# Optimization experiments

Measured on AMD Instinct MI355X. Metric: run time of the kernel, lower is better.

## Reference

```python
import jax, jax.numpy as jnp
import numpy as np

# Module config
SIZE = (2, 2)
B, H, W, C = 16, 64, 64, 256


def setup_inputs() -> dict:
    key = jax.random.key(0)
    updates = jax.random.normal(key, (B, H, W, C), dtype=jnp.float32)
    OH, OW = H * SIZE[0], W * SIZE[1]
    # argmax-style mask: flat index into [OH, OW, C] (per-batch), pointing at the
    # top-left element of each pooling window (structure of max_pool_with_argmax)
    h = jnp.arange(H, dtype=jnp.int64)[:, None, None] * SIZE[0]   # [H,1,1]
    w = jnp.arange(W, dtype=jnp.int64)[None, :, None] * SIZE[1]   # [1,W,1]
    c = jnp.arange(C, dtype=jnp.int64)[None, None, :]             # [1,1,C]
    mask = (h * OW + w) * C + c                                   # [H,W,C]
    mask = jnp.broadcast_to(mask, (B, H, W, C))
    return {"updates": updates, "mask": mask}


def reference(updates, mask):
    # Faithful MaxUnpooling2D: scatter pooled values into upsampled output at
    # the positions given by the (per-batch flat) argmax mask; rest are zeros.
    Bv, Hv, Wv, Cv = updates.shape
    OH, OW = Hv * SIZE[0], Wv * SIZE[1]
    flat = OH * OW * Cv
    out = jnp.zeros((Bv, flat), dtype=updates.dtype)
    # tf.scatter_nd sums duplicates into a zero tensor; indices here are unique
    out = out.at[jnp.arange(Bv)[:, None], mask.reshape(Bv, -1)].add(
        updates.reshape(Bv, -1)
    )
    return out.reshape(Bv, OH, OW, Cv)
```

## Files before the change

kernel.cpp:

```cpp
#include <hip/hip_runtime.h>


constexpr int B = 16;
constexpr int H = 64, W = 64, C = 256;
constexpr int IN_PER_BATCH  = H * W * C;
constexpr int OUT_PER_BATCH = (2 * H) * (2 * W) * C;
constexpr long long N_IN = (long long)B * IN_PER_BATCH;

__global__ void unpool_scatter_kernel(const float* __restrict__ updates,
                                      const int* __restrict__ mask,
                                      float* __restrict__ out) {
    long long i = (long long)blockIdx.x * blockDim.x + threadIdx.x;
    if (i >= N_IN) return;
    int b = (int)(i >> 20);
    int m = mask[i];
    out[(long long)b * OUT_PER_BATCH + m] = updates[i];
}

extern "C" void kernel_launch(void* const* d_in, const int* in_sizes, int n_in,
                              void* d_out, int out_size, void* d_ws, size_t ws_size,
                              hipStream_t stream) {
    const float* updates = (const float*)d_in[0];
    const int*   mask    = (const int*)d_in[1];
    float*       out     = (float*)d_out;

    hipMemsetAsync(out, 0, (size_t)out_size * sizeof(float), stream);

    const int block = 256;
    const int grid  = (int)((N_IN + block - 1) / block);
    unpool_scatter_kernel<<<grid, block, 0, stream>>>(updates, mask, out);
}
```

Baseline: 350.6 us.

## Replace memset plus scatter with a fused per-window gather that writes every output

Drops the separate zero-fill memset and the scattered store. Each thread now owns one pooling window for four channels and writes all four output positions with 128-bit nontemporal stores, putting either the matched update or zero. This removes the extra full pass over the output and the uncoalesced scatter writes. In exchange it assumes each mask index falls inside its own 2x2 window and matching channel, which is true for argmax-style masks but not for arbitrary scatter indices.

```diff
diff --git a/kernel.cpp b/kernel.cpp
--- a/kernel.cpp
+++ b/kernel.cpp
@@ -3,30 +3,54 @@
 
 constexpr int B = 16;
 constexpr int H = 64, W = 64, C = 256;
-constexpr int IN_PER_BATCH  = H * W * C;
-constexpr int OUT_PER_BATCH = (2 * H) * (2 * W) * C;
-constexpr long long N_IN = (long long)B * IN_PER_BATCH;
+constexpr int OH = 2 * H, OW = 2 * W;
+constexpr long long OUT_PER_BATCH = (long long)OH * OW * C;
+constexpr int N_THREADS = B * H * W * (C / 4);
 
-__global__ void unpool_scatter_kernel(const float* __restrict__ updates,
-                                      const int* __restrict__ mask,
-                                      float* __restrict__ out) {
-    long long i = (long long)blockIdx.x * blockDim.x + threadIdx.x;
-    if (i >= N_IN) return;
-    int b = (int)(i >> 20);
-    int m = mask[i];
-    out[(long long)b * OUT_PER_BATCH + m] = updates[i];
+typedef float f32x4 __attribute__((ext_vector_type(4)));
+typedef int   i32x4 __attribute__((ext_vector_type(4)));
+
+__global__ __launch_bounds__(256) void unpool_gather_kernel(
+    const f32x4* __restrict__ upd4,
+    const i32x4* __restrict__ mask4,
+    float* __restrict__ out) {
+    int i = blockIdx.x * blockDim.x + threadIdx.x;
+    if (i >= N_THREADS) return;
+
+    int c0 = (i & 63) << 2;
+    int w  = (i >> 6) & 63;
+    int h  = (i >> 12) & 63;
+    int b  = i >> 18;
+
+    i32x4 m = mask4[i];
+    f32x4 u = upd4[i];
+
+    float* obase = out + (long long)b * OUT_PER_BATCH;
+    int oh = h << 1, ow = w << 1;
+
+#pragma unroll
+    for (int dy = 0; dy < 2; ++dy) {
+#pragma unroll
+        for (int dx = 0; dx < 2; ++dx) {
+            int flat = ((oh + dy) * OW + (ow + dx)) * C + c0;
+            f32x4 r;
+            r.x = (m.x == flat)     ? u.x : 0.0f;
+            r.y = (m.y == flat + 1) ? u.y : 0.0f;
+            r.z = (m.z == flat + 2) ? u.z : 0.0f;
+            r.w = (m.w == flat + 3) ? u.w : 0.0f;
+            __builtin_nontemporal_store(r, (f32x4*)(obase + flat));
+        }
+    }
 }
 
 extern "C" void kernel_launch(void* const* d_in, const int* in_sizes, int n_in,
                               void* d_out, int out_size, void* d_ws, size_t ws_size,
                               hipStream_t stream) {
-    const float* updates = (const float*)d_in[0];
-    const int*   mask    = (const int*)d_in[1];
-    float*       out     = (float*)d_out;
-
-    hipMemsetAsync(out, 0, (size_t)out_size * sizeof(float), stream);
+    const f32x4* upd4  = (const f32x4*)d_in[0];
+    const i32x4* mask4 = (const i32x4*)d_in[1];
+    float*       out   = (float*)d_out;
 
     const int block = 256;
-    const int grid  = (int)((N_IN + block - 1) / block);
-    unpool_scatter_kernel<<<grid, block, 0, stream>>>(updates, mask, out);
+    const int grid  = N_THREADS / block;
+    unpool_gather_kernel<<<grid, block, 0, stream>>>(upd4, mask4, out);
 }
```

New measurement: 360.4 us. +2.8%, slower.
